# Kernel optimization log

Measured on AMD Instinct MI355X. Metric: run time of the kernel, lower is better.

## Reference

```python
import jax, jax.numpy as jnp
import numpy as np

MLOG32 = float(np.log(32.0))


def _maxpool(x, k):
    # F.max_pool2d(stride=1, padding=k//2) pads with -inf, matching init value
    pad = k // 2
    return jax.lax.reduce_window(x, -jnp.inf, jax.lax.max, (1, 1, k, k), (1, 1, 1, 1),
                                 ((0, 0), (0, 0), (pad, pad), (pad, pad)))


def _minpool(x, k):
    return -_maxpool(-x, k)


def _local_sum(x, k):
    # conv2d with all-ones kxk kernel, zero padding, same spatial size
    pad = k // 2
    return jax.lax.reduce_window(x, 0.0, jax.lax.add, (1, 1, k, k), (1, 1, 1, 1),
                                 ((0, 0), (0, 0), (pad, pad), (pad, pad)))


def _conv3(x, kern):
    # torch conv2d == cross-correlation == lax conv (no kernel flip)
    return jax.lax.conv_general_dilated(x, kern, (1, 1), ((1, 1), (1, 1)),
                                        dimension_numbers=('NCHW', 'OIHW', 'NCHW'))


def _otsu(gray, bins=32):
    # vectorized per-batch Otsu threshold; gray in [0,1]
    B, _, H, W = gray.shape
    v = gray.reshape(B, -1)
    idx = jnp.clip((v * bins).astype(jnp.int32), 0, bins - 1)  # histc semantics, v==1 -> last bin
    hist = jax.vmap(lambda i: jnp.bincount(i, length=bins))(idx).astype(gray.dtype)
    p = hist / (H * W + 1e-6)
    xs = jnp.linspace(0.0, 1.0, bins, dtype=gray.dtype)
    omega = jnp.cumsum(p, axis=1)
    mu = jnp.cumsum(p * xs[None, :], axis=1)
    mu_t = mu[:, -1:]
    sigma_b2 = (mu_t * omega - mu) ** 2 / (omega * (1.0 - omega) + 1e-8)
    kbest = jnp.argmax(sigma_b2, axis=1)
    edges = jnp.linspace(0.0, 1.0, bins + 1, dtype=gray.dtype)
    return edges[kbest].reshape(B, 1, 1, 1)


def _concept_maps(image_rgb, cell_dilate=10, k_local=9):
    r, g, b = image_rgb[:, 0:1], image_rgb[:, 1:2], image_rgb[:, 2:3]
    gray = jnp.clip(0.5 * (0.299 * r + 0.587 * g + 0.114 * b + 1.0), 0.0, 1.0)
    thr = _otsu(gray)
    nuc = (gray <= thr).astype(gray.dtype)
    # morphological open+close, k=3
    e = _minpool(nuc, 3)
    d = _maxpool(e, 3)
    d = _maxpool(d, 3)
    e2 = _minpool(d, 3)
    nuc = (e2 > 0.5).astype(gray.dtype)
    er = _minpool(nuc, 3)
    boundary = jnp.maximum(nuc - er, 0.0)
    lap_k = jnp.array([[0, 1, 0], [1, -4, 1], [0, 1, 0]], dtype=gray.dtype).reshape(1, 1, 3, 3)
    lap = jnp.abs(_conv3(nuc, lap_k))
    den = _local_sum(boundary, 5) + 1e-6
    roughness = lap * boundary / den
    kx = jnp.array([[1, 0, -1], [2, 0, -2], [1, 0, -1]], dtype=gray.dtype).reshape(1, 1, 3, 3)
    ky = jnp.array([[1, 2, 1], [0, 0, 0], [-1, -2, -1]], dtype=gray.dtype).reshape(1, 1, 3, 3)
    gx = _conv3(gray, kx)
    gy = _conv3(gray, ky)
    ang = jnp.arctan2(gy, gx)
    den_orient = _local_sum(jnp.ones_like(gray), k_local) + 1e-6
    ms = _local_sum(jnp.sin(ang), k_local) / den_orient
    mc = _local_sum(jnp.cos(ang), k_local) / den_orient
    circ_var = 1.0 - jnp.sqrt(ms ** 2 + mc ** 2 + 1e-6)
    kd = cell_dilate if cell_dilate % 2 == 1 else cell_dilate + 1  # force odd
    cell = jnp.minimum(_maxpool(nuc, kd), 1.0)
    A_n = _local_sum(nuc, k_local)
    A_c = jnp.maximum(_local_sum(cell, k_local) - A_n, 1.0)
    nc = A_n / A_c
    g2 = _local_sum(gray * gray, k_local) / den_orient
    g1 = _local_sum(gray, k_local) / den_orient
    ent_like = jnp.log1p(jnp.maximum(g2 - g1 * g1, 0.0))
    z_maps = jnp.concatenate([roughness, circ_var, nc, ent_like], axis=1)
    return z_maps, nuc


def _energy_forward(image_rgb, cal_a, cal_b, alpha_logits, tau_p, Ht, Wt):
    z_maps, nuc = _concept_maps(image_rgb)
    z0 = jnp.log1p(jnp.maximum(z_maps[:, 0:1], 0.0))
    z1 = jnp.clip(z_maps[:, 1:2], 0.0, 1.0)
    z2 = jnp.log1p(jnp.maximum(z_maps[:, 2:3], 0.0))
    z3 = jnp.clip(z_maps[:, 3:4], 0.0, MLOG32)
    z_stable = jnp.concatenate([z0, z1, z2, z3], axis=1)
    z_cal = jax.nn.softplus(cal_a)[None, :, None, None] * z_stable + cal_b[None, :, None, None]
    alpha = jax.nn.softmax(alpha_logits)[None, :, None, None]
    E = jnp.sum(alpha * z_cal, axis=1, keepdims=True)
    B = E.shape[0]
    if (E.shape[2], E.shape[3]) != (Ht, Wt):
        E_t = jax.image.resize(E, (B, 1, Ht, Wt), method='linear')
    else:
        E_t = E
    tau = 0.2 + jax.nn.softplus(tau_p)
    A = jax.nn.softmax((-E_t / tau).reshape(B, 1, Ht * Wt), axis=-1).reshape(B, 1, Ht, Wt)
    return A, z_maps, nuc, E_t


def setup_inputs() -> dict:
    key = jax.random.key(0)
    k1, k2, k3, k4 = jax.random.split(key, 4)
    B, H, W = 16, 512, 512
    image_rgb = 2.0 * jax.random.uniform(k1, (B, 3, H, W), dtype=jnp.float32) - 1.0
    cal_a = 1.0 + 0.1 * jax.random.normal(k2, (4,), jnp.float32)
    cal_b = 0.1 * jax.random.normal(k3, (4,), jnp.float32)
    alpha_logits = 0.1 * jax.random.normal(k4, (4,), jnp.float32)
    tau_p = jnp.float32(0.5)
    return {"image_rgb": image_rgb, "cal_a": cal_a, "cal_b": cal_b,
            "alpha_logits": alpha_logits, "tau_p": tau_p, "target_h": 512, "target_w": 512}


def reference(image_rgb, cal_a, cal_b, alpha_logits, tau_p, target_h, target_w):
    return _energy_forward(image_rgb, cal_a, cal_b, alpha_logits, tau_p, int(target_h), int(target_w))
```

## Files before the change

kernel.cpp:

```cpp
#include <hip/hip_runtime.h>
#include <math.h>
#include <stdint.h>

#define HW 512
#define IMG (HW*HW)
#define MLOG32f 3.4657359027997265f

__device__ __forceinline__ float grayf(float r, float g, float b) {
    float t = __fadd_rn(__fadd_rn(__fmul_rn(0.299f, r), __fmul_rn(0.587f, g)), __fmul_rn(0.114f, b));
    float s = __fmul_rn(0.5f, __fadd_rn(t, 1.0f));
    return fminf(fmaxf(s, 0.0f), 1.0f);
}

__device__ __forceinline__ float softplusf(float x) {
    return fmaxf(x, 0.0f) + log1pf(expf(-fabsf(x)));
}

__device__ __forceinline__ float frcp(float x)  { return __builtin_amdgcn_rcpf(x); }
__device__ __forceinline__ float frsq(float x)  { return __builtin_amdgcn_rsqf(x); }
__device__ __forceinline__ float flog1p(float x){ return __logf(1.0f + x); }

__device__ __forceinline__ uint64_t kmask(int lo, int hi) {
    return (1ull << hi) - (1ull << lo);
}

__global__ __launch_bounds__(256) void k_gray_hist(const float* __restrict__ img,
                                                   float* __restrict__ gray,
                                                   int* __restrict__ hist) {
    __shared__ int lh[32];
    int tid = threadIdx.x;
    int b = blockIdx.y;
    if (tid < 32) lh[tid] = 0;
    __syncthreads();
    const float4* rp = (const float4*)(img + (size_t)b * 3 * IMG);
    const float4* gp = (const float4*)(img + (size_t)b * 3 * IMG + IMG);
    const float4* bp = (const float4*)(img + (size_t)b * 3 * IMG + 2 * IMG);
    float4* op = (float4*)(gray + (size_t)b * IMG);
    int i = blockIdx.x * 256 + tid;
    float4 r = rp[i], g = gp[i], bb = bp[i];
    float4 o;
    o.x = grayf(r.x, g.x, bb.x);
    o.y = grayf(r.y, g.y, bb.y);
    o.z = grayf(r.z, g.z, bb.z);
    o.w = grayf(r.w, g.w, bb.w);
    op[i] = o;
    int idx[4];
    idx[0] = min(max((int)(o.x * 32.0f), 0), 31);
    idx[1] = min(max((int)(o.y * 32.0f), 0), 31);
    idx[2] = min(max((int)(o.z * 32.0f), 0), 31);
    idx[3] = min(max((int)(o.w * 32.0f), 0), 31);
    int lane = tid & 63;
    int bin = lane & 31;
    int cnt = 0;
    #pragma unroll
    for (int e = 0; e < 4; e++) {
        int v = idx[e];
        unsigned long long m0 = __ballot((v & 1)  != 0);
        unsigned long long m1 = __ballot((v & 2)  != 0);
        unsigned long long m2 = __ballot((v & 4)  != 0);
        unsigned long long m3 = __ballot((v & 8)  != 0);
        unsigned long long m4 = __ballot((v & 16) != 0);
        unsigned long long mm = (bin & 1)  ? m0 : ~m0;
        mm &= (bin & 2)  ? m1 : ~m1;
        mm &= (bin & 4)  ? m2 : ~m2;
        mm &= (bin & 8)  ? m3 : ~m3;
        mm &= (bin & 16) ? m4 : ~m4;
        cnt += __popcll(mm);
    }
    if (lane < 32) atomicAdd(&lh[bin], cnt);
    __syncthreads();
    if (tid < 32) atomicAdd(&hist[b * 32 + tid], lh[tid]);
}

__global__ void k_otsu_sc(const int* __restrict__ hist,
                          const float* __restrict__ cal_a, const float* __restrict__ cal_b,
                          const float* __restrict__ alpha_logits, const float* __restrict__ tau_p,
                          float* __restrict__ thr, float* __restrict__ sc, int B) {
    int tid = threadIdx.x;
    if (tid < B) {
        const int* h = hist + tid * 32;
        float omega[32], mu[32];
        float co = 0.0f, cm = 0.0f;
        for (int k = 0; k < 32; k++) {
            float pk = (float)h[k] * (1.0f / 262144.0f);
            float xs = (float)((double)k / 31.0);
            co += pk;
            cm += pk * xs;
            omega[k] = co; mu[k] = cm;
        }
        float mu_t = mu[31];
        float best = -1e30f; int kb = 0;
        for (int k = 0; k < 32; k++) {
            float t = mu_t * omega[k] - mu[k];
            float sb = (t * t) / (omega[k] * (1.0f - omega[k]) + 1e-8f);
            if (sb > best) { best = sb; kb = k; }
        }
        thr[tid] = (float)kb * 0.03125f;
    }
    if (tid == 63) {
        float al[4];
        float m = -1e30f;
        for (int c = 0; c < 4; c++) { al[c] = alpha_logits[c]; m = fmaxf(m, al[c]); }
        float e[4]; float s = 0.0f;
        for (int c = 0; c < 4; c++) { e[c] = expf(al[c] - m); s += e[c]; }
        float bias = 0.0f;
        for (int c = 0; c < 4; c++) {
            float alpha = e[c] / s;
            sc[c] = alpha * softplusf(cal_a[c]);
            bias += alpha * cal_b[c];
        }
        sc[4] = bias;
        float tau = 0.2f + softplusf(tau_p[0]);
        sc[5] = tau;
        sc[6] = -1.0f / tau;
    }
}

__global__ __launch_bounds__(256) void k_thresh(const float* __restrict__ gray,
                                                const float* __restrict__ thr,
                                                uint32_t* __restrict__ packed) {
    int b = blockIdx.y;
    int i = blockIdx.x * 256 + threadIdx.x;
    float t = thr[b];
    float v = gray[(size_t)b * IMG + i];
    unsigned long long m = __ballot(v <= t);
    if ((threadIdx.x & 63) == 0)
        *(uint64_t*)&packed[(size_t)b * 8192 + (i >> 5)] = m;
}

__global__ __launch_bounds__(256) void k_morph(const uint32_t* __restrict__ p0,
                                               uint32_t* __restrict__ pn) {
    __shared__ uint64_t s0[40], s1[40];
    int tid = threadIdx.x, b = blockIdx.z;
    int x0 = blockIdx.x * 32, y0 = blockIdx.y * 32;
    int w0 = x0 >> 5;
    const uint32_t* pb = p0 + (size_t)b * 8192;
    int xlo = (x0 == 0) ? 4 : 0;
    int xhi = (x0 == 480) ? 36 : 40;
    uint64_t mwin = kmask(xlo, xhi);

    if (tid < 40) {
        int y = y0 - 4 + tid;
        uint64_t v = 0;
        if ((unsigned)y < (unsigned)HW) {
            const uint32_t* rowp = pb + y * 16;
            uint64_t wm = (w0 > 0)  ? rowp[w0 - 1] : 0;
            uint64_t wc = rowp[w0];
            uint64_t wp = (w0 < 15) ? rowp[w0 + 1] : 0;
            v = ((wm >> 28) | (wc << 4) | (wp << 36)) & kmask(0, 40);
        }
        s0[tid] = v;
    }
    __syncthreads();
    if (tid >= 1 && tid < 39) {
        uint64_t e = ~0ull;
        for (int dq = -1; dq <= 1; dq++) {
            int q = tid + dq;
            int y = y0 - 4 + q;
            uint64_t m = ((unsigned)y < (unsigned)HW) ? mwin : 0;
            uint64_t v = s0[q] | ~m;
            e &= v & (v << 1) & (v >> 1);
        }
        s1[tid] = e;
    }
    __syncthreads();
    if (tid >= 2 && tid < 38) {
        uint64_t d = 0;
        uint64_t me = kmask(1, 39);
        for (int dq = -1; dq <= 1; dq++) {
            int q = tid + dq;
            int y = y0 - 4 + q;
            uint64_t m = ((unsigned)y < (unsigned)HW) ? (mwin & me) : 0;
            uint64_t v = s1[q] & m;
            d |= v | (v << 1) | (v >> 1);
        }
        s0[tid] = d;
    }
    __syncthreads();
    if (tid >= 3 && tid < 37) {
        uint64_t d = 0;
        uint64_t me = kmask(2, 38);
        for (int dq = -1; dq <= 1; dq++) {
            int q = tid + dq;
            int y = y0 - 4 + q;
            uint64_t m = ((unsigned)y < (unsigned)HW) ? (mwin & me) : 0;
            uint64_t v = s0[q] & m;
            d |= v | (v << 1) | (v >> 1);
        }
        s1[tid] = d;
    }
    __syncthreads();
    if (tid >= 4 && tid < 36) {
        uint64_t e = ~0ull;
        uint64_t me = kmask(3, 37);
        for (int dq = -1; dq <= 1; dq++) {
            int q = tid + dq;
            int y = y0 - 4 + q;
            uint64_t m = ((unsigned)y < (unsigned)HW) ? (mwin & me) : 0;
            uint64_t v = s1[q] | ~m;
            e &= v & (v << 1) & (v >> 1);
        }
        s0[tid] = e;
    }
    __syncthreads();
    if (tid < 32) {
        int y = y0 + tid;
        pn[(size_t)b * 8192 + y * 16 + w0] = (uint32_t)(s0[tid + 4] >> 4);
    }
}

__global__ __launch_bounds__(256) void k_maps(const float* __restrict__ gray,
                                              const uint32_t* __restrict__ pn,
                                              float* __restrict__ zmap,
                                              float* __restrict__ nucf,
                                              float* __restrict__ Eout,
                                              const float* __restrict__ sc,
                                              float* __restrict__ expsum) {
    __shared__ __align__(16) char smem[30912];
    __shared__ uint64_t nrow[50], ehr[50], dilh[50], bnd[36], cell[40];
    float* gt  = (float*)smem;
    float* st  = (float*)(smem + 7232);
    float* ct  = (float*)(smem + 13792);
    float* rs0 = (float*)(smem + 20352);
    float* rs1 = (float*)(smem + 25632);
    int* rs_n = (int*)smem;
    int* rs_c = (int*)(smem + 5120);
    int* rs_b = (int*)(smem + 10240);
    float* red = (float*)(smem + 16384);

    int tid = threadIdx.x, b = blockIdx.z;
    int x0 = blockIdx.x * 32, y0 = blockIdx.y * 32;
    int w0 = x0 >> 5;
    const float* gb = gray + (size_t)b * IMG;
    const uint32_t* pb = pn + (size_t)b * 8192;
    int xlo = (x0 == 0) ? 9 : 0;
    int xhi = (x0 == 480) ? 41 : 50;
    uint64_t mwin = kmask(xlo, xhi);

    for (int i = tid; i < 42 * 42; i += 256) {
        int ly = i / 42, lx = i % 42;
        int gy = y0 + ly - 5, gx = x0 + lx - 5;
        gt[ly * 43 + lx] = (gy >= 0 && gy < HW && gx >= 0 && gx < HW) ? gb[gy * HW + gx] : 0.0f;
    }
    if (tid < 50) {
        int y = y0 - 9 + tid;
        uint64_t v = 0;
        if ((unsigned)y < (unsigned)HW) {
            const uint32_t* rowp = pb + y * 16;
            uint64_t wm = (w0 > 0)  ? rowp[w0 - 1] : 0;
            uint64_t wc = rowp[w0];
            uint64_t wp = (w0 < 15) ? rowp[w0 + 1] : 0;
            v = ((wm >> 23) | (wc << 9) | (wp << 41)) & kmask(0, 50);
        }
        nrow[tid] = v;
    }
    __syncthreads();

    if (tid < 50) {
        uint64_t v = nrow[tid];
        uint64_t d = v | (v << 1) | (v >> 1);
        d = d | (d << 2) | (d >> 2);
        d = d | (d << 2) | (d >> 2);
        dilh[tid] = d;
    }
    if (tid >= 6 && tid < 44) {
        int y = y0 - 9 + tid;
        uint64_t m = ((unsigned)y < (unsigned)HW) ? mwin : 0;
        uint64_t v = nrow[tid] | ~m;
        ehr[tid] = v & (v << 1) & (v >> 1);
    }
    for (int i = tid; i < 1600; i += 256) {
        int ly = i / 40, lx = i % 40;
        int gy = y0 + ly - 4, gx = x0 + lx - 4;
        float s = 0.0f, c = 0.0f;
        if (gy >= 0 && gy < HW && gx >= 0 && gx < HW) {
            float a00 = gt[ly * 43 + lx],       a01 = gt[ly * 43 + lx + 1],       a02 = gt[ly * 43 + lx + 2];
            float a10 = gt[(ly + 1) * 43 + lx],                                   a12 = gt[(ly + 1) * 43 + lx + 2];
            float a20 = gt[(ly + 2) * 43 + lx], a21 = gt[(ly + 2) * 43 + lx + 1], a22 = gt[(ly + 2) * 43 + lx + 2];
            float gxv = (a00 - a02) + 2.0f * (a10 - a12) + (a20 - a22);
            float gyv = (a00 + 2.0f * a01 + a02) - (a20 + 2.0f * a21 + a22);
            float r2 = gxv * gxv + gyv * gyv;
            if (r2 > 0.0f) { float ir = frsq(r2); s = gyv * ir; c = gxv * ir; }
            else { s = 0.0f; c = 1.0f; }
        }
        st[ly * 41 + lx] = s; ct[ly * 41 + lx] = c;
    }
    __syncthreads();

    if (tid < 36) {
        int r = tid + 7;
        uint64_t er = ehr[r - 1] & ehr[r] & ehr[r + 1];
        bnd[tid] = nrow[r] & ~er;
    }
    if (tid < 40) {
        int r = tid + 5;
        int y = y0 - 4 + tid;
        uint64_t c = 0;
        for (int d = -5; d <= 5; d++) c |= dilh[r + d];
        uint64_t m = ((unsigned)y < (unsigned)HW) ? mwin : 0;
        cell[tid] = c & m;
    }
    for (int i = tid; i < 320; i += 256) {
        int ly = i >> 3, c0 = (i & 7) << 2;
        int base = ly * 41 + c0;
        float sa[12], ca[12];
        #pragma unroll
        for (int j = 0; j < 12; j++) { sa[j] = st[base + j]; ca[j] = ct[base + j]; }
        float ss = sa[0]+sa[1]+sa[2]+sa[3]+sa[4]+sa[5]+sa[6]+sa[7]+sa[8];
        float cs = ca[0]+ca[1]+ca[2]+ca[3]+ca[4]+ca[5]+ca[6]+ca[7]+ca[8];
        int ob = ly * 33 + c0;
        rs0[ob] = ss; rs1[ob] = cs;
        #pragma unroll
        for (int q = 1; q < 4; q++) {
            ss += sa[8 + q] - sa[q - 1];
            cs += ca[8 + q] - ca[q - 1];
            rs0[ob + q] = ss; rs1[ob + q] = cs;
        }
    }
    __syncthreads();

    int p = tid & 31, py0 = (tid >> 5) << 2;
    int gx = x0 + p;
    float cntx = (float)(min(gx + 4, HW - 1) - max(gx - 4, 0) + 1);
    float z1v[4], z3v[4];
    {
        float s[12], c[12];
        #pragma unroll
        for (int j = 0; j < 12; j++) { s[j] = rs0[(py0 + j) * 33 + p]; c[j] = rs1[(py0 + j) * 33 + p]; }
        float ss = s[0]+s[1]+s[2]+s[3]+s[4]+s[5]+s[6]+s[7]+s[8];
        float cs = c[0]+c[1]+c[2]+c[3]+c[4]+c[5]+c[6]+c[7]+c[8];
        #pragma unroll
        for (int q = 0; q < 4; q++) {
            int gy = y0 + py0 + q;
            float cnty = (float)(min(gy + 4, HW - 1) - max(gy - 4, 0) + 1);
            float iden = frcp(cnty * cntx + 1e-6f);
            float ms = ss * iden, mc = cs * iden;
            z1v[q] = 1.0f - sqrtf(ms * ms + mc * mc + 1e-6f);
            if (q < 3) { ss += s[9 + q] - s[q]; cs += c[9 + q] - c[q]; }
        }
    }
    __syncthreads();

    for (int i = tid; i < 320; i += 256) {
        int ly = i >> 3, c0 = (i & 7) << 2;
        int base = (ly + 1) * 43 + c0 + 1;
        float v[12];
        #pragma unroll
        for (int j = 0; j < 12; j++) v[j] = gt[base + j];
        float gs = v[0]+v[1]+v[2]+v[3]+v[4]+v[5]+v[6]+v[7]+v[8];
        float g2 = v[0]*v[0]+v[1]*v[1]+v[2]*v[2]+v[3]*v[3]+v[4]*v[4]+v[5]*v[5]+v[6]*v[6]+v[7]*v[7]+v[8]*v[8];
        int ob = ly * 33 + c0;
        rs0[ob] = gs; rs1[ob] = g2;
        #pragma unroll
        for (int q = 1; q < 4; q++) {
            gs += v[8 + q] - v[q - 1];
            g2 += v[8 + q] * v[8 + q] - v[q - 1] * v[q - 1];
            rs0[ob + q] = gs; rs1[ob + q] = g2;
        }
    }
    __syncthreads();

    {
        float s[12], c[12];
        #pragma unroll
        for (int j = 0; j < 12; j++) { s[j] = rs0[(py0 + j) * 33 + p]; c[j] = rs1[(py0 + j) * 33 + p]; }
        float gs = s[0]+s[1]+s[2]+s[3]+s[4]+s[5]+s[6]+s[7]+s[8];
        float g2 = c[0]+c[1]+c[2]+c[3]+c[4]+c[5]+c[6]+c[7]+c[8];
        #pragma unroll
        for (int q = 0; q < 4; q++) {
            int gy = y0 + py0 + q;
            float cnty = (float)(min(gy + 4, HW - 1) - max(gy - 4, 0) + 1);
            float iden = frcp(cnty * cntx + 1e-6f);
            float g1 = gs * iden, gq = g2 * iden;
            z3v[q] = flog1p(fmaxf(gq - g1 * g1, 0.0f));
            if (q < 3) { gs += s[9 + q] - s[q]; g2 += c[9 + q] - c[q]; }
        }
    }
    __syncthreads();

    for (int i = tid; i < 40 * 32; i += 256) {
        int rr = i >> 5, pp = i & 31;
        rs_n[rr * 32 + pp] = __popcll((nrow[rr + 5] >> (pp + 5)) & 0x1FFull);
        rs_c[rr * 32 + pp] = __popcll((cell[rr]     >> (pp + 5)) & 0x1FFull);
    }
    for (int i = tid; i < 36 * 32; i += 256) {
        int rr = i >> 5, pp = i & 31;
        rs_b[rr * 32 + pp] = __popcll((bnd[rr] >> (pp + 7)) & 0x1Full);
    }
    __syncthreads();

    float w0f = sc[0], w1f = sc[1], w2f = sc[2], w3f = sc[3], bias = sc[4], ntau = sc[6];
    float* z0p = zmap + ((size_t)b * 4 + 0) * IMG;
    float* z1p = zmap + ((size_t)b * 4 + 1) * IMG;
    float* z2p = zmap + ((size_t)b * 4 + 2) * IMG;
    float* z3p = zmap + ((size_t)b * 4 + 3) * IMG;
    float* Ep  = Eout + (size_t)b * IMG;
    float* np  = nucf + (size_t)b * IMG;
    float acc = 0.0f;
    {
        int nn[12], cc[12], bb8[8];
        #pragma unroll
        for (int j = 0; j < 12; j++) { nn[j] = rs_n[(py0 + j) * 32 + p]; cc[j] = rs_c[(py0 + j) * 32 + p]; }
        #pragma unroll
        for (int j = 0; j < 8; j++) bb8[j] = rs_b[(py0 + j) * 32 + p];
        int An = nn[0]+nn[1]+nn[2]+nn[3]+nn[4]+nn[5]+nn[6]+nn[7]+nn[8];
        int Ac = cc[0]+cc[1]+cc[2]+cc[3]+cc[4]+cc[5]+cc[6]+cc[7]+cc[8];
        int db = bb8[0]+bb8[1]+bb8[2]+bb8[3]+bb8[4];
        int kk = p + 9;
        #pragma unroll
        for (int q = 0; q < 4; q++) {
            int py = py0 + q;
            int r = py + 9;
            uint64_t rowc = nrow[r];
            int cbit = (int)((rowc >> kk) & 1);
            int nb4  = (int)((nrow[r - 1] >> kk) & 1) + (int)((nrow[r + 1] >> kk) & 1)
                     + (int)((rowc >> (kk - 1)) & 1) + (int)((rowc >> (kk + 1)) & 1);
            int lap = nb4 - 4 * cbit; lap = lap < 0 ? -lap : lap;
            int bc  = (int)((bnd[py + 2] >> kk) & 1);
            float rough = (float)(lap * bc) * frcp((float)db + 1e-6f);
            float z2 = (float)An * frcp(fmaxf((float)(Ac - An), 1.0f));
            float z0s = flog1p(fmaxf(rough, 0.0f));
            float z1s = fminf(fmaxf(z1v[q], 0.0f), 1.0f);
            float z2s = flog1p(fmaxf(z2, 0.0f));
            float z3s = fminf(fmaxf(z3v[q], 0.0f), MLOG32f);
            float E = w0f * z0s + w1f * z1s + w2f * z2s + w3f * z3s + bias;
            int gy = y0 + py;
            size_t o = (size_t)gy * HW + x0 + p;
            z0p[o] = rough;
            z1p[o] = z1v[q];
            z2p[o] = z2;
            z3p[o] = z3v[q];
            Ep[o]  = E;
            np[o]  = (float)cbit;
            acc += __expf(E * ntau);
            if (q < 3) {
                An += nn[9 + q] - nn[q];
                Ac += cc[9 + q] - cc[q];
                db += bb8[5 + q] - bb8[q];
            }
        }
    }
    for (int off = 32; off > 0; off >>= 1) acc += __shfl_down(acc, off, 64);
    if ((tid & 63) == 0) red[tid >> 6] = acc;
    __syncthreads();
    if (tid == 0) atomicAdd(&expsum[b], red[0] + red[1] + red[2] + red[3]);
}

__global__ __launch_bounds__(256) void k_softmaxA(const float* __restrict__ E,
                                                  float* __restrict__ A,
                                                  const float* __restrict__ sc,
                                                  const float* __restrict__ expsum) {
    int b = blockIdx.y;
    int i = blockIdx.x * 256 + threadIdx.x;
    float ntau = sc[6];
    float invS = 1.0f / expsum[b];
    const float4* Ep = (const float4*)(E + (size_t)b * IMG);
    float4* Ap = (float4*)(A + (size_t)b * IMG);
    float4 e = Ep[i];
    float4 o;
    o.x = __expf(e.x * ntau) * invS;
    o.y = __expf(e.y * ntau) * invS;
    o.z = __expf(e.z * ntau) * invS;
    o.w = __expf(e.w * ntau) * invS;
    Ap[i] = o;
}

extern "C" void kernel_launch(void* const* d_in, const int* in_sizes, int n_in,
                              void* d_out, int out_size, void* d_ws, size_t ws_size,
                              hipStream_t stream) {
    const float* img   = (const float*)d_in[0];
    const float* cal_a = (const float*)d_in[1];
    const float* cal_b = (const float*)d_in[2];
    const float* alpha = (const float*)d_in[3];
    const float* tau_p = (const float*)d_in[4];
    int B = in_sizes[0] / (3 * IMG);

    float* out  = (float*)d_out;
    float* A    = out;
    float* zmap = out + (size_t)B * IMG;
    float* nuc  = out + (size_t)B * IMG * 5;
    float* E    = out + (size_t)B * IMG * 6;
    float* gray = A;

    int*      hist    = (int*)d_ws;
    float*    expsum  = (float*)d_ws + B * 32;
    float*    thr     = expsum + B;
    float*    sc      = thr + B;
    uint32_t* packed0 = (uint32_t*)d_ws + 1024;
    uint32_t* packedN = packed0 + (size_t)B * 8192;

    hipMemsetAsync(d_ws, 0, (size_t)(B * 32 + B) * 4, stream);
    k_gray_hist<<<dim3(IMG / 1024, B), 256, 0, stream>>>(img, gray, hist);
    k_otsu_sc<<<1, 64, 0, stream>>>(hist, cal_a, cal_b, alpha, tau_p, thr, sc, B);
    k_thresh<<<dim3(IMG / 256, B), 256, 0, stream>>>(gray, thr, packed0);
    dim3 tg(HW / 32, HW / 32, B);
    k_morph<<<tg, 256, 0, stream>>>(packed0, packedN);
    k_maps<<<tg, 256, 0, stream>>>(gray, packedN, zmap, nuc, E, sc, expsum);
    k_softmaxA<<<dim3(IMG / 1024, B), 256, 0, stream>>>(E, A, sc, expsum);
}
```

Baseline: 247.9 us.

## Fuse morphology into maps kernel with warp-specialized bitmask pipeline and packed smem

Removes the separate k_morph launch. One wavefront of the k_maps block now recomputes the open/close morphology on a wider 58-row halo, using only compiler fences and no block barriers. The other three wavefronts load the gray tile with float4 loads at the same time. The Sobel orientation is now computed inline from the gray tile in a sliding window rather than staged in smem. Running-sum buffers are transposed into interleaved float2, and popcount row sums are packed as bytes, cutting LDS footprint and traffic. This trades a small amount of redundant halo bit work for one fewer launch, less global traffic and lower LDS use, at the cost of a more complex single-wave dependency chain.

```diff
diff --git a/kernel.cpp b/kernel.cpp
--- a/kernel.cpp
+++ b/kernel.cpp
@@ -4,7 +4,9 @@
 
 #define HW 512
 #define IMG (HW*HW)
+#define GS 52
 #define MLOG32f 3.4657359027997265f
+#define WFENCE() __asm__ __volatile__("" ::: "memory")
 
 __device__ __forceinline__ float grayf(float r, float g, float b) {
     float t = __fadd_rn(__fadd_rn(__fmul_rn(0.299f, r), __fmul_rn(0.587f, g)), __fmul_rn(0.114f, b));
@@ -128,193 +130,181 @@
         *(uint64_t*)&packed[(size_t)b * 8192 + (i >> 5)] = m;
 }
 
-__global__ __launch_bounds__(256) void k_morph(const uint32_t* __restrict__ p0,
-                                               uint32_t* __restrict__ pn) {
-    __shared__ uint64_t s0[40], s1[40];
-    int tid = threadIdx.x, b = blockIdx.z;
-    int x0 = blockIdx.x * 32, y0 = blockIdx.y * 32;
-    int w0 = x0 >> 5;
-    const uint32_t* pb = p0 + (size_t)b * 8192;
-    int xlo = (x0 == 0) ? 4 : 0;
-    int xhi = (x0 == 480) ? 36 : 40;
-    uint64_t mwin = kmask(xlo, xhi);
-
-    if (tid < 40) {
-        int y = y0 - 4 + tid;
-        uint64_t v = 0;
-        if ((unsigned)y < (unsigned)HW) {
-            const uint32_t* rowp = pb + y * 16;
-            uint64_t wm = (w0 > 0)  ? rowp[w0 - 1] : 0;
-            uint64_t wc = rowp[w0];
-            uint64_t wp = (w0 < 15) ? rowp[w0 + 1] : 0;
-            v = ((wm >> 28) | (wc << 4) | (wp << 36)) & kmask(0, 40);
-        }
-        s0[tid] = v;
-    }
-    __syncthreads();
-    if (tid >= 1 && tid < 39) {
-        uint64_t e = ~0ull;
-        for (int dq = -1; dq <= 1; dq++) {
-            int q = tid + dq;
-            int y = y0 - 4 + q;
-            uint64_t m = ((unsigned)y < (unsigned)HW) ? mwin : 0;
-            uint64_t v = s0[q] | ~m;
-            e &= v & (v << 1) & (v >> 1);
-        }
-        s1[tid] = e;
-    }
-    __syncthreads();
-    if (tid >= 2 && tid < 38) {
-        uint64_t d = 0;
-        uint64_t me = kmask(1, 39);
-        for (int dq = -1; dq <= 1; dq++) {
-            int q = tid + dq;
-            int y = y0 - 4 + q;
-            uint64_t m = ((unsigned)y < (unsigned)HW) ? (mwin & me) : 0;
-            uint64_t v = s1[q] & m;
-            d |= v | (v << 1) | (v >> 1);
-        }
-        s0[tid] = d;
-    }
-    __syncthreads();
-    if (tid >= 3 && tid < 37) {
-        uint64_t d = 0;
-        uint64_t me = kmask(2, 38);
-        for (int dq = -1; dq <= 1; dq++) {
-            int q = tid + dq;
-            int y = y0 - 4 + q;
-            uint64_t m = ((unsigned)y < (unsigned)HW) ? (mwin & me) : 0;
-            uint64_t v = s0[q] & m;
-            d |= v | (v << 1) | (v >> 1);
-        }
-        s1[tid] = d;
-    }
-    __syncthreads();
-    if (tid >= 4 && tid < 36) {
-        uint64_t e = ~0ull;
-        uint64_t me = kmask(3, 37);
-        for (int dq = -1; dq <= 1; dq++) {
-            int q = tid + dq;
-            int y = y0 - 4 + q;
-            uint64_t m = ((unsigned)y < (unsigned)HW) ? (mwin & me) : 0;
-            uint64_t v = s1[q] | ~m;
-            e &= v & (v << 1) & (v >> 1);
-        }
-        s0[tid] = e;
-    }
-    __syncthreads();
-    if (tid < 32) {
-        int y = y0 + tid;
-        pn[(size_t)b * 8192 + y * 16 + w0] = (uint32_t)(s0[tid + 4] >> 4);
-    }
-}
-
 __global__ __launch_bounds__(256) void k_maps(const float* __restrict__ gray,
-                                              const uint32_t* __restrict__ pn,
+                                              const uint32_t* __restrict__ p0,
                                               float* __restrict__ zmap,
                                               float* __restrict__ nucf,
                                               float* __restrict__ Eout,
                                               const float* __restrict__ sc,
                                               float* __restrict__ expsum) {
-    __shared__ __align__(16) char smem[30912];
-    __shared__ uint64_t nrow[50], ehr[50], dilh[50], bnd[36], cell[40];
-    float* gt  = (float*)smem;
-    float* st  = (float*)(smem + 7232);
-    float* ct  = (float*)(smem + 13792);
-    float* rs0 = (float*)(smem + 20352);
-    float* rs1 = (float*)(smem + 25632);
-    int* rs_n = (int*)smem;
-    int* rs_c = (int*)(smem + 5120);
-    int* rs_b = (int*)(smem + 10240);
-    float* red = (float*)(smem + 16384);
+    __shared__ __align__(16) char smem[23008];
+    float*    gt   = (float*)smem;
+    float2*   rsP  = (float2*)(smem + 8736);
+    uint64_t* nrow = (uint64_t*)(smem + 20256);
+    uint64_t* dilh = nrow + 50;
+    uint64_t* ehr  = dilh + 50;
+    uint64_t* bnd  = ehr + 50;
+    uint64_t* cell = bnd + 36;
+    uint64_t* m0   = cell + 40;
+    uint64_t* m1   = m0 + 58;
+    int*      rs_nPT = (int*)smem;
+    int*      rs_cPT = (int*)(smem + 1408);
+    int*      rs_bPT = (int*)(smem + 2816);
+    float*    red  = (float*)(smem + 22992);
 
     int tid = threadIdx.x, b = blockIdx.z;
     int x0 = blockIdx.x * 32, y0 = blockIdx.y * 32;
     int w0 = x0 >> 5;
     const float* gb = gray + (size_t)b * IMG;
-    const uint32_t* pb = pn + (size_t)b * 8192;
-    int xlo = (x0 == 0) ? 9 : 0;
-    int xhi = (x0 == 480) ? 41 : 50;
-    uint64_t mwin = kmask(xlo, xhi);
-
-    for (int i = tid; i < 42 * 42; i += 256) {
-        int ly = i / 42, lx = i % 42;
-        int gy = y0 + ly - 5, gx = x0 + lx - 5;
-        gt[ly * 43 + lx] = (gy >= 0 && gy < HW && gx >= 0 && gx < HW) ? gb[gy * HW + gx] : 0.0f;
-    }
-    if (tid < 50) {
-        int y = y0 - 9 + tid;
-        uint64_t v = 0;
-        if ((unsigned)y < (unsigned)HW) {
-            const uint32_t* rowp = pb + y * 16;
-            uint64_t wm = (w0 > 0)  ? rowp[w0 - 1] : 0;
-            uint64_t wc = rowp[w0];
-            uint64_t wp = (w0 < 15) ? rowp[w0 + 1] : 0;
-            v = ((wm >> 23) | (wc << 9) | (wp << 41)) & kmask(0, 50);
-        }
-        nrow[tid] = v;
-    }
-    __syncthreads();
-
-    if (tid < 50) {
-        uint64_t v = nrow[tid];
-        uint64_t d = v | (v << 1) | (v >> 1);
-        d = d | (d << 2) | (d >> 2);
-        d = d | (d << 2) | (d >> 2);
-        dilh[tid] = d;
-    }
-    if (tid >= 6 && tid < 44) {
-        int y = y0 - 9 + tid;
-        uint64_t m = ((unsigned)y < (unsigned)HW) ? mwin : 0;
-        uint64_t v = nrow[tid] | ~m;
-        ehr[tid] = v & (v << 1) & (v >> 1);
-    }
-    for (int i = tid; i < 1600; i += 256) {
-        int ly = i / 40, lx = i % 40;
-        int gy = y0 + ly - 4, gx = x0 + lx - 4;
-        float s = 0.0f, c = 0.0f;
-        if (gy >= 0 && gy < HW && gx >= 0 && gx < HW) {
-            float a00 = gt[ly * 43 + lx],       a01 = gt[ly * 43 + lx + 1],       a02 = gt[ly * 43 + lx + 2];
-            float a10 = gt[(ly + 1) * 43 + lx],                                   a12 = gt[(ly + 1) * 43 + lx + 2];
-            float a20 = gt[(ly + 2) * 43 + lx], a21 = gt[(ly + 2) * 43 + lx + 1], a22 = gt[(ly + 2) * 43 + lx + 2];
-            float gxv = (a00 - a02) + 2.0f * (a10 - a12) + (a20 - a22);
-            float gyv = (a00 + 2.0f * a01 + a02) - (a20 + 2.0f * a21 + a22);
-            float r2 = gxv * gxv + gyv * gyv;
-            if (r2 > 0.0f) { float ir = frsq(r2); s = gyv * ir; c = gxv * ir; }
-            else { s = 0.0f; c = 1.0f; }
-        }
-        st[ly * 41 + lx] = s; ct[ly * 41 + lx] = c;
-    }
-    __syncthreads();
-
-    if (tid < 36) {
-        int r = tid + 7;
-        uint64_t er = ehr[r - 1] & ehr[r] & ehr[r + 1];
-        bnd[tid] = nrow[r] & ~er;
-    }
-    if (tid < 40) {
-        int r = tid + 5;
-        int y = y0 - 4 + tid;
-        uint64_t c = 0;
-        for (int d = -5; d <= 5; d++) c |= dilh[r + d];
-        uint64_t m = ((unsigned)y < (unsigned)HW) ? mwin : 0;
-        cell[tid] = c & m;
-    }
+    const uint32_t* pb = p0 + (size_t)b * 8192;
+
+    if (tid >= 64) {
+        for (int s = tid - 64; s < 504; s += 192) {
+            int r = s / 12, c4 = s - r * 12;
+            int gy = y0 + r - 5;
+            int gxf = (x0 >> 2) + c4 - 2;
+            float4 v = make_float4(0.f, 0.f, 0.f, 0.f);
+            if ((unsigned)gy < (unsigned)HW && (unsigned)gxf < 128u)
+                v = *(const float4*)(gb + gy * HW + (gxf << 2));
+            *(float4*)&gt[r * GS + (c4 << 2)] = v;
+        }
+    } else {
+        int lane = tid;
+        uint64_t mcol = ~0ull;
+        if (x0 == 0)   mcol &= ~((1ull << 13) - 1);
+        if (x0 == 480) mcol = (1ull << 45) - 1;
+        if (lane < 58) {
+            int gy = y0 - 13 + lane;
+            uint64_t v = 0;
+            if ((unsigned)gy < (unsigned)HW) {
+                const uint32_t* rowp = pb + gy * 16;
+                uint64_t wm = (w0 > 0)  ? rowp[w0 - 1] : 0;
+                uint64_t wc = rowp[w0];
+                uint64_t wp = (w0 < 15) ? rowp[w0 + 1] : 0;
+                v = (wm >> 19) | (wc << 13) | (wp << 45);
+            }
+            m0[lane] = v;
+        }
+        WFENCE();
+        if (lane >= 1 && lane < 57) {
+            uint64_t e = ~0ull;
+            #pragma unroll
+            for (int dt = -1; dt <= 1; dt++) {
+                int q = lane + dt;
+                int gy = y0 - 13 + q;
+                uint64_t vv = ((unsigned)gy < (unsigned)HW) ? (m0[q] | ~mcol) : ~0ull;
+                e &= vv & (vv << 1) & (vv >> 1);
+            }
+            m1[lane] = e;
+        }
+        WFENCE();
+        if (lane >= 2 && lane < 56) {
+            uint64_t d = 0;
+            #pragma unroll
+            for (int dt = -1; dt <= 1; dt++) {
+                int q = lane + dt;
+                int gy = y0 - 13 + q;
+                uint64_t vv = ((unsigned)gy < (unsigned)HW) ? (m1[q] & mcol) : 0;
+                d |= vv | (vv << 1) | (vv >> 1);
+            }
+            m0[lane] = d;
+        }
+        WFENCE();
+        if (lane >= 3 && lane < 55) {
+            uint64_t d = 0;
+            #pragma unroll
+            for (int dt = -1; dt <= 1; dt++) {
+                int q = lane + dt;
+                int gy = y0 - 13 + q;
+                uint64_t vv = ((unsigned)gy < (unsigned)HW) ? (m0[q] & mcol) : 0;
+                d |= vv | (vv << 1) | (vv >> 1);
+            }
+            m1[lane] = d;
+        }
+        WFENCE();
+        if (lane >= 4 && lane < 54) {
+            uint64_t e = ~0ull;
+            #pragma unroll
+            for (int dt = -1; dt <= 1; dt++) {
+                int q = lane + dt;
+                int gy = y0 - 13 + q;
+                uint64_t vv = ((unsigned)gy < (unsigned)HW) ? (m1[q] | ~mcol) : ~0ull;
+                e &= vv & (vv << 1) & (vv >> 1);
+            }
+            m0[lane] = e;
+        }
+        WFENCE();
+        if (lane < 50) {
+            int gy = y0 - 9 + lane;
+            uint64_t v = 0;
+            if ((unsigned)gy < (unsigned)HW)
+                v = ((m0[lane + 4] & mcol) >> 4) & ((1ull << 50) - 1);
+            nrow[lane] = v;
+        }
+        WFENCE();
+        uint64_t mwin = kmask(x0 == 0 ? 9 : 0, x0 == 480 ? 41 : 50);
+        if (lane < 50) {
+            uint64_t v = nrow[lane];
+            uint64_t d = v | (v << 1) | (v >> 1);
+            d = d | (d << 2) | (d >> 2);
+            d = d | (d << 2) | (d >> 2);
+            dilh[lane] = d;
+        }
+        if (lane >= 6 && lane < 44) {
+            int y = y0 - 9 + lane;
+            uint64_t m = ((unsigned)y < (unsigned)HW) ? mwin : 0;
+            uint64_t v = nrow[lane] | ~m;
+            ehr[lane] = v & (v << 1) & (v >> 1);
+        }
+        WFENCE();
+        if (lane < 36) {
+            int r = lane + 7;
+            uint64_t er = ehr[r - 1] & ehr[r] & ehr[r + 1];
+            bnd[lane] = nrow[r] & ~er;
+        }
+        if (lane < 40) {
+            int r = lane + 5;
+            int y = y0 - 4 + lane;
+            uint64_t c = 0;
+            #pragma unroll
+            for (int d = -5; d <= 5; d++) c |= dilh[r + d];
+            uint64_t m = ((unsigned)y < (unsigned)HW) ? mwin : 0;
+            cell[lane] = c & m;
+        }
+    }
+    __syncthreads();
+
     for (int i = tid; i < 320; i += 256) {
         int ly = i >> 3, c0 = (i & 7) << 2;
-        int base = ly * 41 + c0;
+        int gyb = y0 + ly - 4;
+        bool rowok = (unsigned)gyb < (unsigned)HW;
+        int gx0 = x0 + c0 - 4;
+        int base = ly * GS + c0 + 3;
+        float a0p = gt[base],          a1p = gt[base + GS],          a2p = gt[base + 2 * GS];
+        float a0q = gt[base + 1],      a1q = gt[base + GS + 1],      a2q = gt[base + 2 * GS + 1];
         float sa[12], ca[12];
         #pragma unroll
-        for (int j = 0; j < 12; j++) { sa[j] = st[base + j]; ca[j] = ct[base + j]; }
+        for (int j = 0; j < 12; j++) {
+            float a0r = gt[base + 2 + j], a1r = gt[base + GS + 2 + j], a2r = gt[base + 2 * GS + 2 + j];
+            float s = 0.0f, c = 0.0f;
+            if (rowok && (unsigned)(gx0 + j) < (unsigned)HW) {
+                float gxv = (a0p - a0r) + 2.0f * (a1p - a1r) + (a2p - a2r);
+                float gyv = (a0p + 2.0f * a0q + a0r) - (a2p + 2.0f * a2q + a2r);
+                float r2 = gxv * gxv + gyv * gyv;
+                if (r2 > 0.0f) { float ir = frsq(r2); s = gyv * ir; c = gxv * ir; }
+                else { s = 0.0f; c = 1.0f; }
+            }
+            sa[j] = s; ca[j] = c;
+            a0p = a0q; a1p = a1q; a2p = a2q;
+            a0q = a0r; a1q = a1r; a2q = a2r;
+        }
         float ss = sa[0]+sa[1]+sa[2]+sa[3]+sa[4]+sa[5]+sa[6]+sa[7]+sa[8];
         float cs = ca[0]+ca[1]+ca[2]+ca[3]+ca[4]+ca[5]+ca[6]+ca[7]+ca[8];
-        int ob = ly * 33 + c0;
-        rs0[ob] = ss; rs1[ob] = cs;
-        #pragma unroll
-        for (int q = 1; q < 4; q++) {
-            ss += sa[8 + q] - sa[q - 1];
-            cs += ca[8 + q] - ca[q - 1];
-            rs0[ob + q] = ss; rs1[ob + q] = cs;
+        #pragma unroll
+        for (int q = 0; q < 4; q++) {
+            float2 t; t.x = ss; t.y = cs;
+            rsP[(c0 + q) * 45 + ly] = t;
+            if (q < 3) { ss += sa[9 + q] - sa[q]; cs += ca[9 + q] - ca[q]; }
         }
     }
     __syncthreads();
@@ -324,11 +314,11 @@
     float cntx = (float)(min(gx + 4, HW - 1) - max(gx - 4, 0) + 1);
     float z1v[4], z3v[4];
     {
-        float s[12], c[12];
-        #pragma unroll
-        for (int j = 0; j < 12; j++) { s[j] = rs0[(py0 + j) * 33 + p]; c[j] = rs1[(py0 + j) * 33 + p]; }
-        float ss = s[0]+s[1]+s[2]+s[3]+s[4]+s[5]+s[6]+s[7]+s[8];
-        float cs = c[0]+c[1]+c[2]+c[3]+c[4]+c[5]+c[6]+c[7]+c[8];
+        float2 v[12];
+        #pragma unroll
+        for (int j = 0; j < 12; j++) v[j] = rsP[p * 45 + py0 + j];
+        float ss = v[0].x+v[1].x+v[2].x+v[3].x+v[4].x+v[5].x+v[6].x+v[7].x+v[8].x;
+        float cs = v[0].y+v[1].y+v[2].y+v[3].y+v[4].y+v[5].y+v[6].y+v[7].y+v[8].y;
         #pragma unroll
         for (int q = 0; q < 4; q++) {
             int gy = y0 + py0 + q;
@@ -336,36 +326,41 @@
             float iden = frcp(cnty * cntx + 1e-6f);
             float ms = ss * iden, mc = cs * iden;
             z1v[q] = 1.0f - sqrtf(ms * ms + mc * mc + 1e-6f);
-            if (q < 3) { ss += s[9 + q] - s[q]; cs += c[9 + q] - c[q]; }
+            if (q < 3) { ss += v[9 + q].x - v[q].x; cs += v[9 + q].y - v[q].y; }
         }
     }
     __syncthreads();
 
     for (int i = tid; i < 320; i += 256) {
         int ly = i >> 3, c0 = (i & 7) << 2;
-        int base = (ly + 1) * 43 + c0 + 1;
+        const float* gr = &gt[(ly + 1) * GS + c0 + 4];
+        float4 A  = *(const float4*)gr;
+        float4 Bv = *(const float4*)(gr + 4);
+        float4 Cv = *(const float4*)(gr + 8);
         float v[12];
-        #pragma unroll
-        for (int j = 0; j < 12; j++) v[j] = gt[base + j];
+        v[0]=A.x;  v[1]=A.y;  v[2]=A.z;  v[3]=A.w;
+        v[4]=Bv.x; v[5]=Bv.y; v[6]=Bv.z; v[7]=Bv.w;
+        v[8]=Cv.x; v[9]=Cv.y; v[10]=Cv.z; v[11]=Cv.w;
         float gs = v[0]+v[1]+v[2]+v[3]+v[4]+v[5]+v[6]+v[7]+v[8];
         float g2 = v[0]*v[0]+v[1]*v[1]+v[2]*v[2]+v[3]*v[3]+v[4]*v[4]+v[5]*v[5]+v[6]*v[6]+v[7]*v[7]+v[8]*v[8];
-        int ob = ly * 33 + c0;
-        rs0[ob] = gs; rs1[ob] = g2;
-        #pragma unroll
-        for (int q = 1; q < 4; q++) {
-            gs += v[8 + q] - v[q - 1];
-            g2 += v[8 + q] * v[8 + q] - v[q - 1] * v[q - 1];
-            rs0[ob + q] = gs; rs1[ob + q] = g2;
+        #pragma unroll
+        for (int q = 0; q < 4; q++) {
+            float2 t; t.x = gs; t.y = g2;
+            rsP[(c0 + q) * 45 + ly] = t;
+            if (q < 3) {
+                gs += v[9 + q] - v[q];
+                g2 += v[9 + q] * v[9 + q] - v[q] * v[q];
+            }
         }
     }
     __syncthreads();
 
     {
-        float s[12], c[12];
-        #pragma unroll
-        for (int j = 0; j < 12; j++) { s[j] = rs0[(py0 + j) * 33 + p]; c[j] = rs1[(py0 + j) * 33 + p]; }
-        float gs = s[0]+s[1]+s[2]+s[3]+s[4]+s[5]+s[6]+s[7]+s[8];
-        float g2 = c[0]+c[1]+c[2]+c[3]+c[4]+c[5]+c[6]+c[7]+c[8];
+        float2 v[12];
+        #pragma unroll
+        for (int j = 0; j < 12; j++) v[j] = rsP[p * 45 + py0 + j];
+        float gs = v[0].x+v[1].x+v[2].x+v[3].x+v[4].x+v[5].x+v[6].x+v[7].x+v[8].x;
+        float g2 = v[0].y+v[1].y+v[2].y+v[3].y+v[4].y+v[5].y+v[6].y+v[7].y+v[8].y;
         #pragma unroll
         for (int q = 0; q < 4; q++) {
             int gy = y0 + py0 + q;
@@ -373,19 +368,32 @@
             float iden = frcp(cnty * cntx + 1e-6f);
             float g1 = gs * iden, gq = g2 * iden;
             z3v[q] = flog1p(fmaxf(gq - g1 * g1, 0.0f));
-            if (q < 3) { gs += s[9 + q] - s[q]; g2 += c[9 + q] - c[q]; }
-        }
-    }
-    __syncthreads();
-
-    for (int i = tid; i < 40 * 32; i += 256) {
-        int rr = i >> 5, pp = i & 31;
-        rs_n[rr * 32 + pp] = __popcll((nrow[rr + 5] >> (pp + 5)) & 0x1FFull);
-        rs_c[rr * 32 + pp] = __popcll((cell[rr]     >> (pp + 5)) & 0x1FFull);
-    }
-    for (int i = tid; i < 36 * 32; i += 256) {
-        int rr = i >> 5, pp = i & 31;
-        rs_b[rr * 32 + pp] = __popcll((bnd[rr] >> (pp + 7)) & 0x1Full);
+            if (q < 3) { gs += v[9 + q].x - v[q].x; g2 += v[9 + q].y - v[q].y; }
+        }
+    }
+    for (int i = tid; i < 320; i += 256) {
+        int rr = i >> 3, p8 = i & 7, pbase = p8 << 2;
+        uint64_t rn = nrow[rr + 5], rc = cell[rr];
+        int vn = 0, vc = 0;
+        #pragma unroll
+        for (int e = 0; e < 4; e++) {
+            int pp = pbase + e;
+            vn |= __popcll((rn >> (pp + 5)) & 0x1FFull) << (e * 8);
+            vc |= __popcll((rc >> (pp + 5)) & 0x1FFull) << (e * 8);
+        }
+        rs_nPT[p8 * 44 + rr] = vn;
+        rs_cPT[p8 * 44 + rr] = vc;
+    }
+    for (int i = tid; i < 288; i += 256) {
+        int rr = i >> 3, p8 = i & 7, pbase = p8 << 2;
+        uint64_t rb = bnd[rr];
+        int vb = 0;
+        #pragma unroll
+        for (int e = 0; e < 4; e++) {
+            int pp = pbase + e;
+            vb |= __popcll((rb >> (pp + 7)) & 0x1Full) << (e * 8);
+        }
+        rs_bPT[p8 * 40 + rr] = vb;
     }
     __syncthreads();
 
@@ -398,14 +406,31 @@
     float* np  = nucf + (size_t)b * IMG;
     float acc = 0.0f;
     {
-        int nn[12], cc[12], bb8[8];
-        #pragma unroll
-        for (int j = 0; j < 12; j++) { nn[j] = rs_n[(py0 + j) * 32 + p]; cc[j] = rs_c[(py0 + j) * 32 + p]; }
-        #pragma unroll
-        for (int j = 0; j < 8; j++) bb8[j] = rs_b[(py0 + j) * 32 + p];
-        int An = nn[0]+nn[1]+nn[2]+nn[3]+nn[4]+nn[5]+nn[6]+nn[7]+nn[8];
-        int Ac = cc[0]+cc[1]+cc[2]+cc[3]+cc[4]+cc[5]+cc[6]+cc[7]+cc[8];
-        int db = bb8[0]+bb8[1]+bb8[2]+bb8[3]+bb8[4];
+        int p8 = p >> 2, sh = (p & 3) << 3;
+        int4 na = *(const int4*)&rs_nPT[p8 * 44 + py0];
+        int4 nb = *(const int4*)&rs_nPT[p8 * 44 + py0 + 4];
+        int4 nc = *(const int4*)&rs_nPT[p8 * 44 + py0 + 8];
+        int4 ka = *(const int4*)&rs_cPT[p8 * 44 + py0];
+        int4 kb = *(const int4*)&rs_cPT[p8 * 44 + py0 + 4];
+        int4 kc = *(const int4*)&rs_cPT[p8 * 44 + py0 + 8];
+        int4 ba = *(const int4*)&rs_bPT[p8 * 40 + py0];
+        int4 bbv = *(const int4*)&rs_bPT[p8 * 40 + py0 + 4];
+        int en[12], ec[12], eb[8];
+        en[0]=na.x; en[1]=na.y; en[2]=na.z; en[3]=na.w;
+        en[4]=nb.x; en[5]=nb.y; en[6]=nb.z; en[7]=nb.w;
+        en[8]=nc.x; en[9]=nc.y; en[10]=nc.z; en[11]=nc.w;
+        ec[0]=ka.x; ec[1]=ka.y; ec[2]=ka.z; ec[3]=ka.w;
+        ec[4]=kb.x; ec[5]=kb.y; ec[6]=kb.z; ec[7]=kb.w;
+        ec[8]=kc.x; ec[9]=kc.y; ec[10]=kc.z; ec[11]=kc.w;
+        eb[0]=ba.x; eb[1]=ba.y; eb[2]=ba.z; eb[3]=ba.w;
+        eb[4]=bbv.x; eb[5]=bbv.y; eb[6]=bbv.z; eb[7]=bbv.w;
+        #pragma unroll
+        for (int j = 0; j < 12; j++) { en[j] = (en[j] >> sh) & 0xFF; ec[j] = (ec[j] >> sh) & 0xFF; }
+        #pragma unroll
+        for (int j = 0; j < 8; j++) eb[j] = (eb[j] >> sh) & 0xFF;
+        int An = en[0]+en[1]+en[2]+en[3]+en[4]+en[5]+en[6]+en[7]+en[8];
+        int Ac = ec[0]+ec[1]+ec[2]+ec[3]+ec[4]+ec[5]+ec[6]+ec[7]+ec[8];
+        int db = eb[0]+eb[1]+eb[2]+eb[3]+eb[4];
         int kk = p + 9;
         #pragma unroll
         for (int q = 0; q < 4; q++) {
@@ -434,9 +459,9 @@
             np[o]  = (float)cbit;
             acc += __expf(E * ntau);
             if (q < 3) {
-                An += nn[9 + q] - nn[q];
-                Ac += cc[9 + q] - cc[q];
-                db += bb8[5 + q] - bb8[q];
+                An += en[9 + q] - en[q];
+                Ac += ec[9 + q] - ec[q];
+                db += eb[5 + q] - eb[q];
             }
         }
     }
@@ -487,14 +512,12 @@
     float*    thr     = expsum + B;
     float*    sc      = thr + B;
     uint32_t* packed0 = (uint32_t*)d_ws + 1024;
-    uint32_t* packedN = packed0 + (size_t)B * 8192;
 
     hipMemsetAsync(d_ws, 0, (size_t)(B * 32 + B) * 4, stream);
     k_gray_hist<<<dim3(IMG / 1024, B), 256, 0, stream>>>(img, gray, hist);
     k_otsu_sc<<<1, 64, 0, stream>>>(hist, cal_a, cal_b, alpha, tau_p, thr, sc, B);
     k_thresh<<<dim3(IMG / 256, B), 256, 0, stream>>>(gray, thr, packed0);
     dim3 tg(HW / 32, HW / 32, B);
-    k_morph<<<tg, 256, 0, stream>>>(packed0, packedN);
-    k_maps<<<tg, 256, 0, stream>>>(gray, packedN, zmap, nuc, E, sc, expsum);
+    k_maps<<<tg, 256, 0, stream>>>(gray, packed0, zmap, nuc, E, sc, expsum);
     k_softmaxA<<<dim3(IMG / 1024, B), 256, 0, stream>>>(E, A, sc, expsum);
 }
```

New measurement: 244.9 us. About the same (-1.2%).
